# Optimization experiments

Measured on AMD Instinct MI355X. Metric: run time of the kernel, lower is better.

The kernel has to match this reference:

```python
import jax, jax.numpy as jnp
import numpy as np


def binarize_det(t):
    # torch: (t - 0.5).sign().add_(1).div_(2)  -> values in {0, 0.5, 1}
    return (jnp.sign(t - 0.5) + 1.0) * 0.5


def setup_inputs() -> dict:
    key = jax.random.key(0)
    k1, k2, k3 = jax.random.split(key, 3)
    B = 4194304
    x = jax.random.uniform(k1, (B, 1, 1, 5), dtype=jnp.float32)
    w_conv = jax.random.uniform(k2, (5, 1, 1, 5), dtype=jnp.float32)   # OIHW
    # init_w: linear weight ~ N(0.5, 0.01)
    w_lin = 0.5 + 0.01 * jax.random.normal(k3, (1, 5), dtype=jnp.float32)
    return {"x": x, "w_conv": w_conv, "w_lin": w_lin}


def reference(x, w_conv, w_lin):
    # BNNConv2d: binarize input and weight, then conv (no bias).
    xb = binarize_det(x)        # [B,1,1,5]
    wcb = binarize_det(w_conv)  # [5,1,1,5]
    # kernel (1,5) with stride 1, pad 0 on a 1x5 input -> 1x1 spatial output;
    # the conv reduces to a dot over the 5-wide window.
    conv_out = jnp.einsum('bk,ok->bo', xb[:, 0, 0, :], wcb[:, 0, 0, :])  # [B,5]
    # Flatten is a no-op on [B,5]. BNNLinear: binarize its input and weight, no bias.
    hb = binarize_det(conv_out)
    wlb = binarize_det(w_lin)
    out = jnp.einsum('bf,of->bo', hb, wlb)  # [B,1]
    return out
```

## Files before the change

kernel.cpp:

```cpp
#include <hip/hip_runtime.h>

__device__ __forceinline__ float binarize(float t) {
    float d = t - 0.5f;
    float s = (d > 0.0f) ? 1.0f : ((d < 0.0f) ? -1.0f : 0.0f);
    return (s + 1.0f) * 0.5f;
}

__global__ __launch_bounds__(256) void Packetbnn_kernel(
    const float* __restrict__ x,
    const float* __restrict__ w_conv,
    const float* __restrict__ w_lin,
    float* __restrict__ out,
    int nquad,
    int nrows)
{
    float wcb[5][5];
#pragma unroll
    for (int o = 0; o < 5; ++o)
#pragma unroll
        for (int k = 0; k < 5; ++k)
            wcb[o][k] = binarize(w_conv[o * 5 + k]);
    float wlb[5];
#pragma unroll
    for (int o = 0; o < 5; ++o) wlb[o] = binarize(w_lin[o]);

    int t = blockIdx.x * blockDim.x + threadIdx.x;
    if (t >= nquad) return;

    const float4* xv = reinterpret_cast<const float4*>(x) + (size_t)t * 5;
    float4 v0 = xv[0], v1 = xv[1], v2 = xv[2], v3 = xv[3], v4 = xv[4];
    float r[20] = {v0.x, v0.y, v0.z, v0.w,
                   v1.x, v1.y, v1.z, v1.w,
                   v2.x, v2.y, v2.z, v2.w,
                   v3.x, v3.y, v3.z, v3.w,
                   v4.x, v4.y, v4.z, v4.w};

    float res[4];
#pragma unroll
    for (int q = 0; q < 4; ++q) {
        float xb[5];
#pragma unroll
        for (int k = 0; k < 5; ++k) xb[k] = binarize(r[q * 5 + k]);
        float acc = 0.0f;
#pragma unroll
        for (int o = 0; o < 5; ++o) {
            float c = 0.0f;
#pragma unroll
            for (int k = 0; k < 5; ++k) c += xb[k] * wcb[o][k];
            acc += binarize(c) * wlb[o];
        }
        res[q] = acc;
    }

    float4 o4 = {res[0], res[1], res[2], res[3]};
    reinterpret_cast<float4*>(out)[t] = o4;

    if (t == 0) {
        for (int row = nquad * 4; row < nrows; ++row) {
            float xb[5];
            for (int k = 0; k < 5; ++k) xb[k] = binarize(x[(size_t)row * 5 + k]);
            float acc = 0.0f;
            for (int o = 0; o < 5; ++o) {
                float c = 0.0f;
                for (int k = 0; k < 5; ++k) c += xb[k] * wcb[o][k];
                acc += binarize(c) * wlb[o];
            }
            out[row] = acc;
        }
    }
}

extern "C" void kernel_launch(void* const* d_in, const int* in_sizes, int n_in,
                              void* d_out, int out_size, void* d_ws, size_t ws_size,
                              hipStream_t stream) {
    const float* x      = (const float*)d_in[0];
    const float* w_conv = (const float*)d_in[1];
    const float* w_lin  = (const float*)d_in[2];
    float* out = (float*)d_out;

    int nrows = out_size;
    int nquad = nrows / 4;
    int threads = 256;
    int blocks = (nquad + threads - 1) / threads;
    if (blocks < 1) blocks = 1;

    Packetbnn_kernel<<<blocks, threads, 0, stream>>>(x, w_conv, w_lin, out,
                                                     nquad, nrows);
}
```

Before: 21.07 us.

## Replace per-row binarized dot products with a 243-entry shared LUT and grid-stride loop

Each block builds a 3^5 lookup table in shared memory that maps every ternary input pattern to its final output. Each row then needs only a ternary index and one LDS read instead of the two binarized matmuls. The launch becomes a persistent grid-stride loop capped at 2048 blocks, and the output is written with nontemporal stores. The kernel reads about 84 MB and is memory-bound, so the compute savings may matter little, and the per-block LUT build adds a sync and setup cost.

```diff
diff --git a/kernel.cpp b/kernel.cpp
--- a/kernel.cpp
+++ b/kernel.cpp
@@ -6,7 +6,14 @@
     return (s + 1.0f) * 0.5f;
 }
 
-__global__ __launch_bounds__(256) void Packetbnn_kernel(
+__device__ __forceinline__ int tri(float v) {
+    float d = v - 0.5f;
+    return (d > 0.0f) ? 2 : ((d < 0.0f) ? 0 : 1);
+}
+
+typedef float f32x4 __attribute__((ext_vector_type(4)));
+
+__global__ __launch_bounds__(256, 8) void Packetbnn_kernel(
     const float* __restrict__ x,
     const float* __restrict__ w_conv,
     const float* __restrict__ w_lin,
@@ -14,58 +21,57 @@
     int nquad,
     int nrows)
 {
-    float wcb[5][5];
-#pragma unroll
-    for (int o = 0; o < 5; ++o)
-#pragma unroll
-        for (int k = 0; k < 5; ++k)
-            wcb[o][k] = binarize(w_conv[o * 5 + k]);
-    float wlb[5];
-#pragma unroll
-    for (int o = 0; o < 5; ++o) wlb[o] = binarize(w_lin[o]);
+    __shared__ float lut[243];
 
-    int t = blockIdx.x * blockDim.x + threadIdx.x;
-    if (t >= nquad) return;
-
-    const float4* xv = reinterpret_cast<const float4*>(x) + (size_t)t * 5;
-    float4 v0 = xv[0], v1 = xv[1], v2 = xv[2], v3 = xv[3], v4 = xv[4];
-    float r[20] = {v0.x, v0.y, v0.z, v0.w,
-                   v1.x, v1.y, v1.z, v1.w,
-                   v2.x, v2.y, v2.z, v2.w,
-                   v3.x, v3.y, v3.z, v3.w,
-                   v4.x, v4.y, v4.z, v4.w};
-
-    float res[4];
-#pragma unroll
-    for (int q = 0; q < 4; ++q) {
+    const int tid = threadIdx.x;
+    if (tid < 243) {
+        int n = tid;
         float xb[5];
 #pragma unroll
-        for (int k = 0; k < 5; ++k) xb[k] = binarize(r[q * 5 + k]);
+        for (int k = 0; k < 5; ++k) { xb[k] = 0.5f * (float)(n % 3); n /= 3; }
         float acc = 0.0f;
 #pragma unroll
         for (int o = 0; o < 5; ++o) {
             float c = 0.0f;
 #pragma unroll
-            for (int k = 0; k < 5; ++k) c += xb[k] * wcb[o][k];
-            acc += binarize(c) * wlb[o];
+            for (int k = 0; k < 5; ++k) c += xb[k] * binarize(w_conv[o * 5 + k]);
+            acc += binarize(c) * binarize(w_lin[o]);
         }
-        res[q] = acc;
+        lut[tid] = acc;
+    }
+    __syncthreads();
+
+    const float4* xv = reinterpret_cast<const float4*>(x);
+    f32x4* ov = reinterpret_cast<f32x4*>(out);
+    const long stride = (long)gridDim.x * blockDim.x;
+
+    for (long t = (long)blockIdx.x * blockDim.x + tid; t < nquad; t += stride) {
+        const float4* p = xv + t * 5;
+        float4 v0 = p[0], v1 = p[1], v2 = p[2], v3 = p[3], v4 = p[4];
+        float r[20] = {v0.x, v0.y, v0.z, v0.w,
+                       v1.x, v1.y, v1.z, v1.w,
+                       v2.x, v2.y, v2.z, v2.w,
+                       v3.x, v3.y, v3.z, v3.w,
+                       v4.x, v4.y, v4.z, v4.w};
+        float res[4];
+#pragma unroll
+        for (int q = 0; q < 4; ++q) {
+            int idx = tri(r[q * 5 + 0])
+                    + 3  * tri(r[q * 5 + 1])
+                    + 9  * tri(r[q * 5 + 2])
+                    + 27 * tri(r[q * 5 + 3])
+                    + 81 * tri(r[q * 5 + 4]);
+            res[q] = lut[idx];
+        }
+        f32x4 o4 = {res[0], res[1], res[2], res[3]};
+        __builtin_nontemporal_store(o4, ov + t);
     }
 
-    float4 o4 = {res[0], res[1], res[2], res[3]};
-    reinterpret_cast<float4*>(out)[t] = o4;
-
-    if (t == 0) {
+    if (blockIdx.x == 0 && tid == 0) {
         for (int row = nquad * 4; row < nrows; ++row) {
-            float xb[5];
-            for (int k = 0; k < 5; ++k) xb[k] = binarize(x[(size_t)row * 5 + k]);
-            float acc = 0.0f;
-            for (int o = 0; o < 5; ++o) {
-                float c = 0.0f;
-                for (int k = 0; k < 5; ++k) c += xb[k] * wcb[o][k];
-                acc += binarize(c) * wlb[o];
-            }
-            out[row] = acc;
+            int idx = 0, w = 1;
+            for (int k = 0; k < 5; ++k) { idx += w * tri(x[(size_t)row * 5 + k]); w *= 3; }
+            out[row] = lut[idx];
         }
     }
 }
@@ -81,8 +87,8 @@
     int nrows = out_size;
     int nquad = nrows / 4;
     int threads = 256;
-    int blocks = (nquad + threads - 1) / threads;
-    if (blocks < 1) blocks = 1;
+    long need = ((long)nquad + threads - 1) / threads;
+    int blocks = (int)(need < 2048 ? (need < 1 ? 1 : need) : 2048);
 
     Packetbnn_kernel<<<blocks, threads, 0, stream>>>(x, w_conv, w_lin, out,
                                                      nquad, nrows);
```

After: 21.67 us. 2.9% more time.
